# Kernel tuning notes

Measured on AMD Instinct MI355X. Metric: run time of the kernel, lower is better.

Reference implementation:

```python
import jax, jax.numpy as jnp
import numpy as np

N_NODES = 10000
N_EDGES = 320000
N_GRAPHS = 64
IN_DIM = 1
HID = 256


def setup_inputs() -> dict:
    key = jax.random.key(0)
    ks = jax.random.split(key, 12)
    s = 1.0 / np.sqrt(HID)
    inp = {
        "x": jax.random.normal(ks[0], (N_NODES, IN_DIM), dtype=jnp.float32),
        "edge_index": jax.random.randint(ks[1], (2, N_EDGES), 0, N_NODES, dtype=jnp.int64),
        "batch": jnp.sort(jax.random.randint(ks[2], (N_NODES,), 0, N_GRAPHS, dtype=jnp.int64)),
        "W_emb": jax.random.normal(ks[3], (IN_DIM, HID), dtype=jnp.float32),
        "b_emb": jnp.zeros((HID,), dtype=jnp.float32),
        "W1a": jax.random.normal(ks[4], (HID, HID), dtype=jnp.float32) * s,
        "b1a": jnp.zeros((HID,), dtype=jnp.float32),
        "W1b": jax.random.normal(ks[5], (HID, HID), dtype=jnp.float32) * s,
        "b1b": jnp.zeros((HID,), dtype=jnp.float32),
        "W2a": jax.random.normal(ks[6], (HID, HID), dtype=jnp.float32) * s,
        "b2a": jnp.zeros((HID,), dtype=jnp.float32),
        "W2b": jax.random.normal(ks[7], (HID, HID), dtype=jnp.float32) * s,
        "b2b": jnp.zeros((HID,), dtype=jnp.float32),
    }
    return inp


def _pointnet_conv(h, src, dst, Wa, ba, Wb, bb):
    # gather x_j -> 2-layer MLP per edge -> scatter-max at dst (PyG aggr='max')
    msg = jax.nn.relu(h[src] @ Wa + ba) @ Wb + bb          # [E, HID]
    agg = jax.ops.segment_max(msg, dst, num_segments=N_NODES)
    # PyG fills nodes with no incoming messages with 0
    return jnp.where(jnp.isneginf(agg), 0.0, agg)


def reference(x, edge_index, batch, W_emb, b_emb, W1a, b1a, W1b, b1b, W2a, b2a, W2b, b2b):
    src, dst = edge_index[0], edge_index[1]
    h = jax.nn.silu(x @ W_emb + b_emb)                     # [N, HID]
    h = h + jax.nn.silu(_pointnet_conv(h, src, dst, W1a, b1a, W1b, b1b))
    h = h + jax.nn.silu(_pointnet_conv(h, src, dst, W2a, b2a, W2b, b2b))
    # global_mean_pool over graphs
    sums = jax.ops.segment_sum(h, batch, num_segments=N_GRAPHS)          # [G, HID]
    cnts = jax.ops.segment_sum(jnp.ones((h.shape[0],), h.dtype), batch, num_segments=N_GRAPHS)
    return sums / jnp.maximum(cnts, 1.0)[:, None]
```

## Files before the change

kernel.cpp:

```cpp
#include <hip/hip_runtime.h>
#include <hip/hip_bf16.h>
#include <math.h>

#define HID 256
#define CAP 128

typedef __attribute__((ext_vector_type(8))) short bf16x8;
typedef __attribute__((ext_vector_type(8))) unsigned short u16x8;
typedef __attribute__((ext_vector_type(4))) float f32x4;

__device__ __forceinline__ float silu_f(float z) {
    return z / (1.0f + __expf(-z));
}
__device__ __forceinline__ unsigned short f2bf(float f) {
    unsigned int u = __float_as_uint(f);
    u = (u + 0x7FFFu + ((u >> 16) & 1u)) >> 16;
    return (unsigned short)u;
}
__device__ __forceinline__ float bf2f(unsigned short b) {
    return __uint_as_float(((unsigned int)b) << 16);
}
__device__ __forceinline__ void max8(float m[8], u16x8 v) {
#pragma unroll
    for (int k = 0; k < 8; ++k) m[k] = fmaxf(m[k], bf2f(v[k]));
}

__global__ __launch_bounds__(256) void k_prep(
    const float* __restrict__ w0, const float* __restrict__ w1,
    const float* __restrict__ w2, const float* __restrict__ w3,
    unsigned short* __restrict__ o0, unsigned short* __restrict__ o1,
    unsigned short* __restrict__ o2, unsigned short* __restrict__ o3,
    int* __restrict__ cnt,
    const int* __restrict__ batch, int* __restrict__ goff,
    int N, int G) {
    __shared__ float ls[64][65];
    int b = blockIdx.x;
    int tid = threadIdx.x;
    if (b < 64) {
        int mat = b >> 4;
        int tile = b & 15;
        int k0 = (tile >> 2) * 64;
        int n0 = (tile & 3) * 64;
        const float* in = (mat == 0) ? w0 : (mat == 1) ? w1 : (mat == 2) ? w2 : w3;
        unsigned short* op = (mat == 0) ? o0 : (mat == 1) ? o1 : (mat == 2) ? o2 : o3;
        int lrb = tid >> 4;
        int lc = (tid & 15) * 4;
#pragma unroll
        for (int p = 0; p < 4; ++p) {
            int lr = p * 16 + lrb;
            float4 v = *(const float4*)(in + (size_t)(k0 + lr) * HID + n0 + lc);
            ls[lr][lc + 0] = v.x; ls[lr][lc + 1] = v.y;
            ls[lr][lc + 2] = v.z; ls[lr][lc + 3] = v.w;
        }
        __syncthreads();
#pragma unroll
        for (int p = 0; p < 4; ++p) {
            int ln = p * 16 + lrb;
            ushort4 q;
            q.x = f2bf(ls[lc + 0][ln]);
            q.y = f2bf(ls[lc + 1][ln]);
            q.z = f2bf(ls[lc + 2][ln]);
            q.w = f2bf(ls[lc + 3][ln]);
            *(ushort4*)(op + (size_t)(n0 + ln) * HID + k0 + lc) = q;
        }
    } else if (b == 64) {
        int g = tid;
        if (g > G) return;
        int lo = 0, hi = N;
        while (lo < hi) {
            int mid = (lo + hi) >> 1;
            if (batch[mid] < g) lo = mid + 1; else hi = mid;
        }
        goff[g] = lo;
    } else {
        int i = (b - 65) * 256 + tid;
        if (i < N) cnt[i] = 0;
    }
}

__global__ __launch_bounds__(256) void k_mlp1f(
    const float* __restrict__ x, const float* __restrict__ Wemb,
    const float* __restrict__ bemb,
    const unsigned short* __restrict__ Wta, const float* __restrict__ ba,
    const unsigned short* __restrict__ Wtb, const float* __restrict__ bbv,
    unsigned short* __restrict__ hb, unsigned short* __restrict__ t2,
    const int* __restrict__ src, const int* __restrict__ dst,
    int* __restrict__ cnt, unsigned short* __restrict__ csr,
    int M, int E, int MT) {
    __shared__ unsigned short As[32][264];
    __shared__ unsigned short t1s[32][264];
    int b = blockIdx.x;
    int tid = threadIdx.x;

    if (b >= MT) {
        int e0 = ((b - MT) * 256 + tid) * 4;
        if (e0 + 3 < E) {
            int4 d4 = *(const int4*)(dst + e0);
            int4 s4 = *(const int4*)(src + e0);
            int p0 = atomicAdd(&cnt[d4.x], 1);
            int p1 = atomicAdd(&cnt[d4.y], 1);
            int p2 = atomicAdd(&cnt[d4.z], 1);
            int p3 = atomicAdd(&cnt[d4.w], 1);
            if (p0 < CAP) csr[d4.x * CAP + p0] = (unsigned short)s4.x;
            if (p1 < CAP) csr[d4.y * CAP + p1] = (unsigned short)s4.y;
            if (p2 < CAP) csr[d4.z * CAP + p2] = (unsigned short)s4.z;
            if (p3 < CAP) csr[d4.w * CAP + p3] = (unsigned short)s4.w;
        } else {
            for (int e = e0; e < E; ++e) {
                int d = dst[e];
                int p = atomicAdd(&cnt[d], 1);
                if (p < CAP) csr[d * CAP + p] = (unsigned short)src[e];
            }
        }
        return;
    }

    int lane = tid & 63;
    int wave = tid >> 6;
    int quad = lane >> 4;
    int r = lane & 15;
    int m0 = b * 32;
    int colw = wave * 64;

    {
        int row = tid >> 3;
        int c0 = (tid & 7) * 32;
        int grow = m0 + row;
        float xv = (grow < M) ? x[grow] : 0.0f;
#pragma unroll
        for (int j = 0; j < 8; ++j) {
            int c = c0 + j * 4;
            ushort4 q;
            q.x = f2bf(silu_f(xv * Wemb[c + 0] + bemb[c + 0]));
            q.y = f2bf(silu_f(xv * Wemb[c + 1] + bemb[c + 1]));
            q.z = f2bf(silu_f(xv * Wemb[c + 2] + bemb[c + 2]));
            q.w = f2bf(silu_f(xv * Wemb[c + 3] + bemb[c + 3]));
            if (grow < M) *(ushort4*)(hb + (size_t)grow * HID + c) = q;
            *(ushort4*)&As[row][c] = q;
        }
        __syncthreads();
    }

    f32x4 acc[2][4];
#pragma unroll
    for (int rt = 0; rt < 2; ++rt)
#pragma unroll
        for (int nt = 0; nt < 4; ++nt) acc[rt][nt] = (f32x4)0.0f;
#pragma unroll
    for (int ks = 0; ks < 8; ++ks) {
        bf16x8 a0 = *(const bf16x8*)&As[r][ks * 32 + quad * 8];
        bf16x8 a1 = *(const bf16x8*)&As[r + 16][ks * 32 + quad * 8];
#pragma unroll
        for (int nt = 0; nt < 4; ++nt) {
            bf16x8 bfr = *(const bf16x8*)(Wta + (size_t)(colw + nt * 16 + r) * HID
                                          + ks * 32 + quad * 8);
            acc[0][nt] = __builtin_amdgcn_mfma_f32_16x16x32_bf16(a0, bfr, acc[0][nt], 0, 0, 0);
            acc[1][nt] = __builtin_amdgcn_mfma_f32_16x16x32_bf16(a1, bfr, acc[1][nt], 0, 0, 0);
        }
    }
#pragma unroll
    for (int nt = 0; nt < 4; ++nt) {
        int col = colw + nt * 16 + r;
        float bv = ba[col];
#pragma unroll
        for (int rt = 0; rt < 2; ++rt)
#pragma unroll
            for (int i = 0; i < 4; ++i) {
                float v = fmaxf(acc[rt][nt][i] + bv, 0.0f);
                t1s[rt * 16 + quad * 4 + i][col] = f2bf(v);
            }
    }
    __syncthreads();

    f32x4 acc2[2][4];
#pragma unroll
    for (int rt = 0; rt < 2; ++rt)
#pragma unroll
        for (int nt = 0; nt < 4; ++nt) acc2[rt][nt] = (f32x4)0.0f;
#pragma unroll
    for (int ks = 0; ks < 8; ++ks) {
        bf16x8 a0 = *(const bf16x8*)&t1s[r][ks * 32 + quad * 8];
        bf16x8 a1 = *(const bf16x8*)&t1s[r + 16][ks * 32 + quad * 8];
#pragma unroll
        for (int nt = 0; nt < 4; ++nt) {
            bf16x8 bfr = *(const bf16x8*)(Wtb + (size_t)(colw + nt * 16 + r) * HID
                                          + ks * 32 + quad * 8);
            acc2[0][nt] = __builtin_amdgcn_mfma_f32_16x16x32_bf16(a0, bfr, acc2[0][nt], 0, 0, 0);
            acc2[1][nt] = __builtin_amdgcn_mfma_f32_16x16x32_bf16(a1, bfr, acc2[1][nt], 0, 0, 0);
        }
    }
#pragma unroll
    for (int nt = 0; nt < 4; ++nt) {
        int col = colw + nt * 16 + r;
        float bv = bbv[col];
#pragma unroll
        for (int rt = 0; rt < 2; ++rt)
#pragma unroll
            for (int i = 0; i < 4; ++i) {
                int row = m0 + rt * 16 + quad * 4 + i;
                if (row < M) t2[(size_t)row * HID + col] = f2bf(acc2[rt][nt][i] + bv);
            }
    }
}

__global__ __launch_bounds__(256) void k_mlp2(
    const unsigned short* __restrict__ Aglob,
    const unsigned short* __restrict__ Wta, const float* __restrict__ ba,
    const unsigned short* __restrict__ Wtb, const float* __restrict__ bbv,
    unsigned short* __restrict__ t2, int M) {
    __shared__ unsigned short t1s[32][264];
    int tid = threadIdx.x;
    int lane = tid & 63;
    int wave = tid >> 6;
    int quad = lane >> 4;
    int r = lane & 15;
    int m0 = blockIdx.x * 32;
    int colw = wave * 64;

    f32x4 acc[2][4];
#pragma unroll
    for (int rt = 0; rt < 2; ++rt)
#pragma unroll
        for (int nt = 0; nt < 4; ++nt) acc[rt][nt] = (f32x4)0.0f;

    int ar0 = m0 + r;        if (ar0 >= M) ar0 = M - 1;
    int ar1 = m0 + 16 + r;   if (ar1 >= M) ar1 = M - 1;

#pragma unroll
    for (int ks = 0; ks < 8; ++ks) {
        bf16x8 a0 = *(const bf16x8*)(Aglob + (size_t)ar0 * HID + ks * 32 + quad * 8);
        bf16x8 a1 = *(const bf16x8*)(Aglob + (size_t)ar1 * HID + ks * 32 + quad * 8);
#pragma unroll
        for (int nt = 0; nt < 4; ++nt) {
            bf16x8 bfr = *(const bf16x8*)(Wta + (size_t)(colw + nt * 16 + r) * HID
                                          + ks * 32 + quad * 8);
            acc[0][nt] = __builtin_amdgcn_mfma_f32_16x16x32_bf16(a0, bfr, acc[0][nt], 0, 0, 0);
            acc[1][nt] = __builtin_amdgcn_mfma_f32_16x16x32_bf16(a1, bfr, acc[1][nt], 0, 0, 0);
        }
    }
#pragma unroll
    for (int nt = 0; nt < 4; ++nt) {
        int col = colw + nt * 16 + r;
        float bv = ba[col];
#pragma unroll
        for (int rt = 0; rt < 2; ++rt)
#pragma unroll
            for (int i = 0; i < 4; ++i) {
                float v = fmaxf(acc[rt][nt][i] + bv, 0.0f);
                t1s[rt * 16 + quad * 4 + i][col] = f2bf(v);
            }
    }
    __syncthreads();

    f32x4 acc2[2][4];
#pragma unroll
    for (int rt = 0; rt < 2; ++rt)
#pragma unroll
        for (int nt = 0; nt < 4; ++nt) acc2[rt][nt] = (f32x4)0.0f;
#pragma unroll
    for (int ks = 0; ks < 8; ++ks) {
        bf16x8 a0 = *(const bf16x8*)&t1s[r][ks * 32 + quad * 8];
        bf16x8 a1 = *(const bf16x8*)&t1s[r + 16][ks * 32 + quad * 8];
#pragma unroll
        for (int nt = 0; nt < 4; ++nt) {
            bf16x8 bfr = *(const bf16x8*)(Wtb + (size_t)(colw + nt * 16 + r) * HID
                                          + ks * 32 + quad * 8);
            acc2[0][nt] = __builtin_amdgcn_mfma_f32_16x16x32_bf16(a0, bfr, acc2[0][nt], 0, 0, 0);
            acc2[1][nt] = __builtin_amdgcn_mfma_f32_16x16x32_bf16(a1, bfr, acc2[1][nt], 0, 0, 0);
        }
    }
#pragma unroll
    for (int nt = 0; nt < 4; ++nt) {
        int col = colw + nt * 16 + r;
        float bv = bbv[col];
#pragma unroll
        for (int rt = 0; rt < 2; ++rt)
#pragma unroll
            for (int i = 0; i < 4; ++i) {
                int row = m0 + rt * 16 + quad * 4 + i;
                if (row < M) t2[(size_t)row * HID + col] = f2bf(acc2[rt][nt][i] + bv);
            }
    }
}

__global__ __launch_bounds__(256) void k_agg(const unsigned short* __restrict__ t2,
                                             const int* __restrict__ cnt,
                                             const unsigned short* __restrict__ csr,
                                             unsigned short* __restrict__ hb, int N) {
    int lane = threadIdx.x & 63;
    int node = (blockIdx.x * blockDim.x + threadIdx.x) >> 6;
    if (node >= N) return;
    int half = lane >> 5;
    int lc = (lane & 31) * 8;
    const unsigned short* base = t2 + lc;

    int deg = cnt[node];
    if (deg > CAP) deg = CAP;
    const unsigned short* rowp = csr + (size_t)node * CAP;
    size_t o = (size_t)node * HID + lc;
    u16x8 hq = *(const u16x8*)(hb + o);

    float m[8];
#pragma unroll
    for (int k = 0; k < 8; ++k) m[k] = -INFINITY;

    int i = 0;
    for (; i + 16 <= deg; i += 16) {
        int s[8];
#pragma unroll
        for (int j = 0; j < 8; ++j) s[j] = rowp[i + 2 * j + half];
        u16x8 v[8];
#pragma unroll
        for (int j = 0; j < 8; ++j) v[j] = *(const u16x8*)(base + (size_t)s[j] * HID);
#pragma unroll
        for (int j = 0; j < 8; ++j) max8(m, v[j]);
    }
    if (i + 8 <= deg) {
        int s[4];
#pragma unroll
        for (int j = 0; j < 4; ++j) s[j] = rowp[i + 2 * j + half];
        u16x8 v[4];
#pragma unroll
        for (int j = 0; j < 4; ++j) v[j] = *(const u16x8*)(base + (size_t)s[j] * HID);
#pragma unroll
        for (int j = 0; j < 4; ++j) max8(m, v[j]);
        i += 8;
    }
    for (; i < deg; i += 2) {
        int idx = i + half; if (idx >= deg) idx = deg - 1;
        int s = rowp[idx];
        u16x8 v = *(const u16x8*)(base + (size_t)s * HID);
        max8(m, v);
    }

#pragma unroll
    for (int k = 0; k < 8; ++k) m[k] = fmaxf(m[k], __shfl_xor(m[k], 32, 64));
    if (deg == 0) {
#pragma unroll
        for (int k = 0; k < 8; ++k) m[k] = 0.0f;
    }

    if (half == 0) {
        u16x8 q;
#pragma unroll
        for (int k = 0; k < 8; ++k) q[k] = f2bf(bf2f(hq[k]) + silu_f(m[k]));
        *(u16x8*)(hb + o) = q;
    }
}

__global__ __launch_bounds__(1024) void k_pool(const unsigned short* __restrict__ hb,
                                               const int* __restrict__ goff,
                                               float* __restrict__ out) {
    __shared__ float part[3][HID];
    int g = blockIdx.x;
    int tid = threadIdx.x;
    int c = tid & 255;
    int chunk = tid >> 8;
    int beg = goff[g], end = goff[g + 1];
    float s = 0.f;
    for (int n = beg + chunk; n < end; n += 4) s += bf2f(hb[(size_t)n * HID + c]);
    if (chunk > 0) part[chunk - 1][c] = s;
    __syncthreads();
    if (chunk == 0) {
        s += part[0][c] + part[1][c] + part[2][c];
        int cnt = end - beg;
        out[g * HID + c] = s / (float)(cnt > 0 ? cnt : 1);
    }
}

extern "C" void kernel_launch(void* const* d_in, const int* in_sizes, int n_in,
                              void* d_out, int out_size, void* d_ws, size_t ws_size,
                              hipStream_t stream) {
    const float* x     = (const float*)d_in[0];
    const int*   ei    = (const int*)d_in[1];
    const int*   batch = (const int*)d_in[2];
    const float* Wemb  = (const float*)d_in[3];
    const float* bemb  = (const float*)d_in[4];
    const float* W1a   = (const float*)d_in[5];
    const float* b1a   = (const float*)d_in[6];
    const float* W1b   = (const float*)d_in[7];
    const float* b1b   = (const float*)d_in[8];
    const float* W2a   = (const float*)d_in[9];
    const float* b2a   = (const float*)d_in[10];
    const float* W2b   = (const float*)d_in[11];
    const float* b2b   = (const float*)d_in[12];
    float* out = (float*)d_out;

    const int N = in_sizes[0];
    const int E = in_sizes[1] / 2;
    const int G = out_size / HID;
    const int* src = ei;
    const int* dst = ei + E;

    char* ws = (char*)d_ws;
    unsigned short* hb   = (unsigned short*)ws; ws += (size_t)N * HID * 2;
    unsigned short* t2   = (unsigned short*)ws; ws += (size_t)N * HID * 2;
    unsigned short* Wt1a = (unsigned short*)ws; ws += (size_t)HID * HID * 2;
    unsigned short* Wt1b = (unsigned short*)ws; ws += (size_t)HID * HID * 2;
    unsigned short* Wt2a = (unsigned short*)ws; ws += (size_t)HID * HID * 2;
    unsigned short* Wt2b = (unsigned short*)ws; ws += (size_t)HID * HID * 2;
    int* cnt  = (int*)ws; ws += (size_t)N * 4;
    int* goff = (int*)ws; ws += (size_t)(G + 1) * 4;
    unsigned short* csr = (unsigned short*)ws; ws += (size_t)N * CAP * 2;

    const int nh = (E + 1023) / 1024;
    const int nz = (N + 255) / 256;
    const int MT = (N + 31) / 32;

    k_prep<<<64 + 1 + nz, 256, 0, stream>>>(W1a, W1b, W2a, W2b,
                                            Wt1a, Wt1b, Wt2a, Wt2b,
                                            cnt, batch, goff, N, G);

    k_mlp1f<<<MT + nh, 256, 0, stream>>>(x, Wemb, bemb, Wt1a, b1a, Wt1b, b1b,
                                         hb, t2, src, dst, cnt, csr, N, E, MT);

    int agg_blocks = (N * 64 + 255) / 256;

    k_agg<<<agg_blocks, 256, 0, stream>>>(t2, cnt, csr, hb, N);

    k_mlp2<<<MT, 256, 0, stream>>>(hb, Wt2a, b2a, Wt2b, b2b, t2, N);

    k_agg<<<agg_blocks, 256, 0, stream>>>(t2, cnt, csr, hb, N);

    k_pool<<<G, 1024, 0, stream>>>(hb, goff, out);
}
```

Before: 202.6 us.

## Build CSR with per-block shared-memory histograms and prefix offsets

Global atomics on the per-node counter for CSR construction are replaced by a two-pass scheme. Each of 64 edge chunks first builds a shared-memory histogram of destinations, a new prefix kernel turns these into per-chunk base offsets, and the fill pass then uses shared atomics plus those bases. This removes contended global atomics but adds a kernel launch, a 64xN offset buffer, and a 40KB shared allocation that is now also reserved by the GEMM blocks of k_mlp1f, which can lower their occupancy. The shared array is hardcoded to 10000 entries, so it relies on N being at most 10000.

```diff
diff --git a/kernel.cpp b/kernel.cpp
--- a/kernel.cpp
+++ b/kernel.cpp
@@ -4,6 +4,7 @@
 
 #define HID 256
 #define CAP 128
+#define FB 64
 
 typedef __attribute__((ext_vector_type(8))) short bf16x8;
 typedef __attribute__((ext_vector_type(8))) unsigned short u16x8;
@@ -30,13 +31,14 @@
     const float* __restrict__ w2, const float* __restrict__ w3,
     unsigned short* __restrict__ o0, unsigned short* __restrict__ o1,
     unsigned short* __restrict__ o2, unsigned short* __restrict__ o3,
-    int* __restrict__ cnt,
+    const int* __restrict__ dst, int* __restrict__ cbase,
     const int* __restrict__ batch, int* __restrict__ goff,
-    int N, int G) {
-    __shared__ float ls[64][65];
+    int N, int G, int E, int chunk) {
+    __shared__ __align__(16) int shp[10000];
     int b = blockIdx.x;
     int tid = threadIdx.x;
     if (b < 64) {
+        float (*ls)[65] = (float(*)[65])shp;
         int mat = b >> 4;
         int tile = b & 15;
         int k0 = (tile >> 2) * 64;
@@ -73,9 +75,38 @@
         }
         goff[g] = lo;
     } else {
-        int i = (b - 65) * 256 + tid;
-        if (i < N) cnt[i] = 0;
-    }
+        int fb = b - 65;
+        int* hist = shp;
+        for (int i = tid; i < N; i += 256) hist[i] = 0;
+        __syncthreads();
+        int e0 = fb * chunk;
+        int e1 = min(E, e0 + chunk);
+        for (int e = e0 + tid * 4; e + 3 < e1; e += 1024) {
+            int4 d4 = *(const int4*)(dst + e);
+            atomicAdd(&hist[d4.x], 1);
+            atomicAdd(&hist[d4.y], 1);
+            atomicAdd(&hist[d4.z], 1);
+            atomicAdd(&hist[d4.w], 1);
+        }
+        int rem = (e1 - e0) & 3;
+        if (tid < rem) atomicAdd(&hist[dst[e1 - rem + tid]], 1);
+        __syncthreads();
+        for (int i = tid; i < N; i += 256) cbase[(size_t)fb * N + i] = hist[i];
+    }
+}
+
+__global__ __launch_bounds__(256) void k_prefix(int* __restrict__ cbase,
+                                                int* __restrict__ cnt, int N) {
+    int d = blockIdx.x * 256 + threadIdx.x;
+    if (d >= N) return;
+    int run = 0;
+#pragma unroll
+    for (int b = 0; b < FB; ++b) {
+        int c = cbase[(size_t)b * N + d];
+        cbase[(size_t)b * N + d] = run;
+        run += c;
+    }
+    cnt[d] = run;
 }
 
 __global__ __launch_bounds__(256) void k_mlp1f(
@@ -85,32 +116,45 @@
     const unsigned short* __restrict__ Wtb, const float* __restrict__ bbv,
     unsigned short* __restrict__ hb, unsigned short* __restrict__ t2,
     const int* __restrict__ src, const int* __restrict__ dst,
-    int* __restrict__ cnt, unsigned short* __restrict__ csr,
-    int M, int E, int MT) {
-    __shared__ unsigned short As[32][264];
-    __shared__ unsigned short t1s[32][264];
+    const int* __restrict__ cbase, unsigned short* __restrict__ csr,
+    int M, int E, int MT, int chunk) {
+    __shared__ __align__(16) int shbuf[10000];
+    unsigned short (*As)[264]  = (unsigned short(*)[264])shbuf;
+    unsigned short (*t1s)[264] = (unsigned short(*)[264])((char*)shbuf + 16896);
     int b = blockIdx.x;
     int tid = threadIdx.x;
 
     if (b >= MT) {
-        int e0 = ((b - MT) * 256 + tid) * 4;
-        if (e0 + 3 < E) {
-            int4 d4 = *(const int4*)(dst + e0);
-            int4 s4 = *(const int4*)(src + e0);
-            int p0 = atomicAdd(&cnt[d4.x], 1);
-            int p1 = atomicAdd(&cnt[d4.y], 1);
-            int p2 = atomicAdd(&cnt[d4.z], 1);
-            int p3 = atomicAdd(&cnt[d4.w], 1);
+        int fb = b - MT;
+        int* hist = shbuf;
+        for (int i = tid; i < M; i += 256) hist[i] = 0;
+        __syncthreads();
+        int e0 = fb * chunk;
+        int e1 = min(E, e0 + chunk);
+        const int* cb = cbase + (size_t)fb * M;
+        for (int e = e0 + tid * 4; e + 3 < e1; e += 1024) {
+            int4 d4 = *(const int4*)(dst + e);
+            int4 s4 = *(const int4*)(src + e);
+            int r0 = atomicAdd(&hist[d4.x], 1);
+            int r1 = atomicAdd(&hist[d4.y], 1);
+            int r2 = atomicAdd(&hist[d4.z], 1);
+            int r3 = atomicAdd(&hist[d4.w], 1);
+            int p0 = cb[d4.x] + r0;
+            int p1 = cb[d4.y] + r1;
+            int p2 = cb[d4.z] + r2;
+            int p3 = cb[d4.w] + r3;
             if (p0 < CAP) csr[d4.x * CAP + p0] = (unsigned short)s4.x;
             if (p1 < CAP) csr[d4.y * CAP + p1] = (unsigned short)s4.y;
             if (p2 < CAP) csr[d4.z * CAP + p2] = (unsigned short)s4.z;
             if (p3 < CAP) csr[d4.w * CAP + p3] = (unsigned short)s4.w;
-        } else {
-            for (int e = e0; e < E; ++e) {
-                int d = dst[e];
-                int p = atomicAdd(&cnt[d], 1);
-                if (p < CAP) csr[d * CAP + p] = (unsigned short)src[e];
-            }
+        }
+        int rem = (e1 - e0) & 3;
+        if (tid < rem) {
+            int e = e1 - rem + tid;
+            int d = dst[e];
+            int r = atomicAdd(&hist[d], 1);
+            int p = cb[d] + r;
+            if (p < CAP) csr[d * CAP + p] = (unsigned short)src[e];
         }
         return;
     }
@@ -399,20 +443,22 @@
     unsigned short* Wt1b = (unsigned short*)ws; ws += (size_t)HID * HID * 2;
     unsigned short* Wt2a = (unsigned short*)ws; ws += (size_t)HID * HID * 2;
     unsigned short* Wt2b = (unsigned short*)ws; ws += (size_t)HID * HID * 2;
-    int* cnt  = (int*)ws; ws += (size_t)N * 4;
-    int* goff = (int*)ws; ws += (size_t)(G + 1) * 4;
+    int* cnt   = (int*)ws; ws += (size_t)N * 4;
+    int* goff  = (int*)ws; ws += (size_t)(G + 1) * 4;
+    int* cbase = (int*)ws; ws += (size_t)FB * N * 4;
     unsigned short* csr = (unsigned short*)ws; ws += (size_t)N * CAP * 2;
 
-    const int nh = (E + 1023) / 1024;
-    const int nz = (N + 255) / 256;
+    const int chunk = (((E + FB - 1) / FB) + 3) & ~3;
     const int MT = (N + 31) / 32;
 
-    k_prep<<<64 + 1 + nz, 256, 0, stream>>>(W1a, W1b, W2a, W2b,
+    k_prep<<<64 + 1 + FB, 256, 0, stream>>>(W1a, W1b, W2a, W2b,
                                             Wt1a, Wt1b, Wt2a, Wt2b,
-                                            cnt, batch, goff, N, G);
-
-    k_mlp1f<<<MT + nh, 256, 0, stream>>>(x, Wemb, bemb, Wt1a, b1a, Wt1b, b1b,
-                                         hb, t2, src, dst, cnt, csr, N, E, MT);
+                                            dst, cbase, batch, goff, N, G, E, chunk);
+
+    k_prefix<<<(N + 255) / 256, 256, 0, stream>>>(cbase, cnt, N);
+
+    k_mlp1f<<<MT + FB, 256, 0, stream>>>(x, Wemb, bemb, Wt1a, b1a, Wt1b, b1b,
+                                         hb, t2, src, dst, cbase, csr, N, E, MT, chunk);
 
     int agg_blocks = (N * 64 + 255) / 256;
 
```

New measurement: 194.7 us. 1.04x faster.
